# Optimization experiments

Hardware: AMD Instinct MI355X
Metric: run time of the kernel (lower is better)

The kernel has to match this reference:

```python
import jax, jax.numpy as jnp
import numpy as np

B, S, HID = 2, 4096, 768
H, DH = 12, 64
FF = 3072
W = 128  # one-sided attention band; window span = 2*W+1
EPS = 1e-12


def _ln(x, g, b):
    m = jnp.mean(x, axis=-1, keepdims=True)
    v = jnp.var(x, axis=-1, keepdims=True)
    return (x - m) * jax.lax.rsqrt(v + EPS) * g + b


def _band_attend(q, k, v, dmask, w):
    # q,k,v: (B,H,S,D) fp32; dmask: (B,S,2w+1) additive key-mask. Returns (B,S,H,D).
    b, h, s, d = q.shape
    nc = s // w
    qc = q.reshape(b, h, nc, w, d)
    pad = ((0, 0), (0, 0), (w, w), (0, 0))
    kp = jnp.pad(k, pad)
    vp = jnp.pad(v, pad)
    win = jnp.arange(nc)[:, None] * w + jnp.arange(3 * w)[None, :]  # (nc, 3w) indices into padded seq
    kc = kp[:, :, win]  # (B,H,nc,3w,D)
    vc = vp[:, :, win]
    s3 = jnp.einsum('bhcxd,bhcyd->bhcxy', qc, kc)  # (B,H,nc,w,3w)
    # extract band: query i in chunk attends keys j in [i, i+2w] of the 3w window
    off = jnp.arange(w)[:, None] + jnp.arange(2 * w + 1)[None, :]  # (w, 2w+1)
    band = jnp.take_along_axis(s3, off[None, None, None], axis=-1)  # (B,H,nc,w,2w+1)
    band = band.reshape(b, h, s, 2 * w + 1)
    keypos = jnp.arange(s)[:, None] + jnp.arange(-w, w + 1)[None, :]
    valid = (keypos >= 0) & (keypos < s)  # mask_invalid_locations
    band = jnp.where(valid[None, None], band, -1e30)
    band = band + dmask[:, None]
    p = jax.nn.softmax(band, axis=-1)
    # scatter probs back to chunk-dense (w, 3w) layout for the PV matmul
    pc = p.reshape(b, h, nc, w, 2 * w + 1)
    j = jnp.arange(3 * w)[None, :] - jnp.arange(w)[:, None]  # (w,3w) offset indices
    ok = (j >= 0) & (j <= 2 * w)
    jcl = jnp.clip(j, 0, 2 * w)
    pdense = jnp.take_along_axis(pc, jcl[None, None, None], axis=-1)  # (B,H,nc,w,3w)
    pdense = jnp.where(ok[None, None, None], pdense, 0.0)
    ctx = jnp.einsum('bhcxy,bhcyd->bhcxd', pdense, vc)  # (B,H,nc,w,D)
    return ctx.reshape(b, h, s, d).transpose(0, 2, 1, 3)


def setup_inputs() -> dict:
    key = jax.random.key(0)
    ks = jax.random.split(key, 8)
    sc = 0.02
    inp = {
        'hidden_states': jax.random.normal(ks[0], (B, S, HID), jnp.float32),
        'attention_mask': jax.random.randint(ks[1], (B, 1, 1, S), 0, 2, jnp.int32),
        'Wq': jax.random.normal(ks[2], (HID, HID), jnp.float32) * sc,
        'bq': jnp.zeros((HID,), jnp.float32),
        'Wk': jax.random.normal(ks[3], (HID, HID), jnp.float32) * sc,
        'bk': jnp.zeros((HID,), jnp.float32),
        'Wv': jax.random.normal(ks[4], (HID, HID), jnp.float32) * sc,
        'bv': jnp.zeros((HID,), jnp.float32),
        'Wd': jax.random.normal(ks[5], (HID, HID), jnp.float32) * sc,
        'bd': jnp.zeros((HID,), jnp.float32),
        'ln1_g': jnp.ones((HID,), jnp.float32),
        'ln1_b': jnp.zeros((HID,), jnp.float32),
        'Wf': jax.random.normal(ks[6], (HID, FF), jnp.float32) * sc,
        'bf': jnp.zeros((FF,), jnp.float32),
        'Wo': jax.random.normal(ks[7], (FF, HID), jnp.float32) * sc,
        'bo': jnp.zeros((HID,), jnp.float32),
        'ln2_g': jnp.ones((HID,), jnp.float32),
        'ln2_b': jnp.zeros((HID,), jnp.float32),
    }
    return inp


def reference(hidden_states, attention_mask, Wq, bq, Wk, bk, Wv, bv, Wd, bd,
              ln1_g, ln1_b, Wf, bf, Wo, bo, ln2_g, ln2_b):
    def heads(x):
        return x.reshape(B, S, H, DH).transpose(0, 2, 1, 3)  # (B,H,S,DH)

    q = heads(hidden_states @ Wq + bq).astype(jnp.float32) / np.float32(np.sqrt(DH))
    k = heads(hidden_states @ Wk + bk).astype(jnp.float32)
    v = heads(hidden_states @ Wv + bv).astype(jnp.float32)

    am = attention_mask.reshape(B, S)
    maskvals = jnp.where(am != 0, -10000.0, 0.0).astype(jnp.float32)  # (B,S)
    mpad = jnp.pad(maskvals, ((0, 0), (W, W)))
    kidx = jnp.arange(S)[:, None] + jnp.arange(2 * W + 1)[None, :]
    dmask = mpad[:, kidx]  # (B,S,2w+1)

    ctx = _band_attend(q, k, v, dmask, W)  # (B,S,H,DH)

    w_d = Wd.reshape(H, DH, HID)
    proj = jnp.einsum('bfnd,ndh->bfh', ctx, w_d) + bd
    attn_out = _ln(hidden_states + proj, ln1_g, ln1_b)

    ff = jax.nn.gelu(attn_out @ Wf + bf, approximate=False)
    ff = ff @ Wo + bo
    return _ln(ff + attn_out, ln2_g, ln2_b)
```

## Files before the change

### kernel.cpp

```cpp
#include <hip/hip_runtime.h>
#include <cstdint>
#include <cstddef>

#define S_LEN 4096
#define HIDD 768
#define NH 12
#define FFD 3072

typedef float f32x4 __attribute__((ext_vector_type(4)));
typedef short s16x8 __attribute__((ext_vector_type(8)));
typedef short s16x4 __attribute__((ext_vector_type(4)));

__device__ __forceinline__ short f2bf(float f) {
  unsigned u = __float_as_uint(f);
  u += 0x7fffu + ((u >> 16) & 1u);
  return (short)(u >> 16);
}
__device__ __forceinline__ float bf2f(short s) {
  return __uint_as_float(((unsigned)(unsigned short)s) << 16);
}

__device__ __forceinline__ void gload16(const short* g, short* l) {
  __builtin_amdgcn_global_load_lds(
      (__attribute__((address_space(1))) void*)(void*)const_cast<short*>(g),
      (__attribute__((address_space(3))) void*)l, 16, 0, 0);
}

__global__ void convx_k(const float* __restrict__ x, short* __restrict__ o) {
  size_t i = (size_t)blockIdx.x * 256 + threadIdx.x;
  float4 f = ((const float4*)x)[i];
  s16x4 v;
  v[0] = f2bf(f.x); v[1] = f2bf(f.y); v[2] = f2bf(f.z); v[3] = f2bf(f.w);
  ((s16x4*)o)[i] = v;
}

__global__ void wtrans_k(const float* __restrict__ Wq, const float* __restrict__ Wk,
                         const float* __restrict__ Wv, const float* __restrict__ Wd,
                         const float* __restrict__ Wf, const float* __restrict__ Wo,
                         short* __restrict__ oq, short* __restrict__ ok_,
                         short* __restrict__ ov, short* __restrict__ od,
                         short* __restrict__ of_, short* __restrict__ oo) {
  __shared__ float tl[64][65];
  int id = blockIdx.x;
  const float* in; short* out; int R, C, tr, tc;
  if (id < 576) {
    int wsel = id / 144; int t = id % 144; tr = t / 12; tc = t % 12; R = 768; C = 768;
    in = wsel == 0 ? Wq : wsel == 1 ? Wk : wsel == 2 ? Wv : Wd;
    out = wsel == 0 ? oq : wsel == 1 ? ok_ : wsel == 2 ? ov : od;
  } else if (id < 1152) {
    int t = id - 576; tr = t / 48; tc = t % 48; R = 768; C = 3072; in = Wf; out = of_;
  } else {
    int t = id - 1152; tr = t / 12; tc = t % 12; R = 3072; C = 768; in = Wo; out = oo;
  }
  int r0 = tr * 64, c0 = tc * 64;
  int tid = threadIdx.x;
  #pragma unroll
  for (int i = 0; i < 16; i++) {
    int idx = i * 256 + tid; int r = idx >> 6, cc = idx & 63;
    tl[r][cc] = in[(size_t)(r0 + r) * C + c0 + cc];
  }
  __syncthreads();
  #pragma unroll
  for (int i = 0; i < 16; i++) {
    int idx = i * 256 + tid; int cc = idx >> 6, rr = idx & 63;
    out[(size_t)(c0 + cc) * R + r0 + rr] = f2bf(tl[rr][cc]);
  }
}

__global__ void vtrans_k(const short* __restrict__ vh, short* __restrict__ vth) {
  __shared__ short tl[64][72];
  int s0 = blockIdx.x * 64; int bh = blockIdx.y;
  int tid = threadIdx.x;
  const short* base = vh + ((size_t)bh << 18);
  #pragma unroll
  for (int i = 0; i < 16; i++) {
    int idx = i * 256 + tid; int r = idx >> 6, cc = idx & 63;
    tl[r][cc] = base[(size_t)(s0 + r) * 64 + cc];
  }
  __syncthreads();
  short* ob = vth + ((size_t)bh << 18);
  #pragma unroll
  for (int i = 0; i < 16; i++) {
    int idx = i * 256 + tid; int dh = idx >> 6, s = idx & 63;
    ob[((size_t)dh << 12) + s0 + s] = tl[s][dh];
  }
}

template <int EPI, int BN>
__global__ void __launch_bounds__(256) gemm_bt(
    const short* __restrict__ A, const short* __restrict__ Bt,
    const float* __restrict__ bias, const float* __restrict__ bias1,
    const float* __restrict__ bias2, const void* __restrict__ resid,
    void* __restrict__ out, int N, int K) {
  constexpr int NT = BN / 32;
  __shared__ __align__(16) short As[2][128 * 64];
  __shared__ __align__(16) short Bs[2][BN * 64];
  const int tid = threadIdx.x;
  const int lane = tid & 63;
  const int w = tid >> 6;
  const int wr = w >> 1, wc = w & 1;
  const int m0 = blockIdx.x * 128, n0 = blockIdx.y * BN;
  const int lr = lane >> 3;
  const int seg = (lane & 7) ^ lr;
  f32x4 acc[4][NT];
  #pragma unroll
  for (int i = 0; i < 4; i++)
    #pragma unroll
    for (int j = 0; j < NT; j++) { acc[i][j][0] = 0.f; acc[i][j][1] = 0.f; acc[i][j][2] = 0.f; acc[i][j][3] = 0.f; }

  const short* Ab = A + (size_t)(m0 + lr) * K + seg * 8;
  const short* Bb = Bt + (size_t)(n0 + lr) * K + seg * 8;

  auto stage = [&](int buf, int k0) {
    #pragma unroll
    for (int i = 0; i < 4; i++) {
      const int ca = w * 4 + i;
      gload16(Ab + (size_t)(ca * 8) * K + k0, &As[buf][ca * 512]);
    }
    #pragma unroll
    for (int i = 0; i < NT; i++) {
      const int cb = w * NT + i;
      gload16(Bb + (size_t)(cb * 8) * K + k0, &Bs[buf][cb * 512]);
    }
  };

  const int nt_k = K >> 6;
  stage(0, 0);
  __syncthreads();
  int cur = 0;
  for (int t = 0; t < nt_k; ++t) {
    if (t + 1 < nt_k) stage(cur ^ 1, (t + 1) << 6);
    const int kc = (lane >> 4) * 8;
    #pragma unroll
    for (int ks = 0; ks < 2; ks++) {
      const int kb = ks * 32 + kc;
      s16x8 af[4], bfr[NT];
      #pragma unroll
      for (int mt = 0; mt < 4; mt++) {
        const int arow = wr * 64 + mt * 16 + (lane & 15);
        af[mt] = *(const s16x8*)&As[cur][arow * 64 + (kb ^ ((arow & 7) << 3))];
      }
      #pragma unroll
      for (int nt = 0; nt < NT; nt++) {
        const int brow = wc * (BN / 2) + nt * 16 + (lane & 15);
        bfr[nt] = *(const s16x8*)&Bs[cur][brow * 64 + (kb ^ ((brow & 7) << 3))];
      }
      #pragma unroll
      for (int mt = 0; mt < 4; mt++)
        #pragma unroll
        for (int nt = 0; nt < NT; nt++)
          acc[mt][nt] = __builtin_amdgcn_mfma_f32_16x16x32_bf16(af[mt], bfr[nt], acc[mt][nt], 0, 0, 0);
    }
    if (t + 1 < nt_k) {
      __syncthreads();
      cur ^= 1;
    }
  }
  #pragma unroll
  for (int nt = 0; nt < NT; nt++) {
    const int col = n0 + wc * (BN / 2) + nt * 16 + (lane & 15);
    if (EPI == 0) {
      const int cwhich = col >= 1536 ? 2 : (col >= 768 ? 1 : 0);
      const int cwi = col - cwhich * 768;
      const float* bsel = cwhich == 0 ? bias : (cwhich == 1 ? bias1 : bias2);
      const float bvv = bsel[cwi];
      const float sc = (cwhich == 0) ? 0.125f : 1.f;
      const int hh = cwi >> 6, dh = cwi & 63;
      short* outp = (short*)out + (size_t)cwhich * ((size_t)8192 * 768);
      #pragma unroll
      for (int mt = 0; mt < 4; mt++) {
        #pragma unroll
        for (int r = 0; r < 4; r++) {
          const int row = m0 + wr * 64 + mt * 16 + (lane >> 4) * 4 + r;
          const int b = row >> 12, s = row & 4095;
          outp[((((size_t)b * NH + hh) * S_LEN + s) << 6) + dh] = f2bf((acc[mt][nt][r] + bvv) * sc);
        }
      }
    } else {
      const float bvv = bias[col];
      #pragma unroll
      for (int mt = 0; mt < 4; mt++) {
        #pragma unroll
        for (int r = 0; r < 4; r++) {
          const int row = m0 + wr * 64 + mt * 16 + (lane >> 4) * 4 + r;
          float v = acc[mt][nt][r] + bvv;
          if (EPI == 1) {
            float u = 0.7978845608f * v * (1.f + 0.044715f * v * v);
            float e = __expf(2.f * u);
            float th = 1.f - 2.f / (e + 1.f);
            float g = 0.5f * v * (1.f + th);
            ((short*)out)[(size_t)row * N + col] = f2bf(g);
          } else if (EPI == 2) {
            ((float*)out)[(size_t)row * N + col] = v + ((const float*)resid)[(size_t)row * N + col];
          } else {
            ((float*)out)[(size_t)row * N + col] = v + bf2f(((const short*)resid)[(size_t)row * N + col]);
          }
        }
      }
    }
  }
}

__global__ void __launch_bounds__(512, 1) attn_k(
    const short* __restrict__ qh, const short* __restrict__ kh,
    const short* __restrict__ vth, const int* __restrict__ am,
    short* __restrict__ ctx) {
  extern __shared__ char smraw[];
  short* Kb = (short*)smraw;
  float* dmw = (float*)(smraw + 55296);
  short* Pb = (short*)(smraw + 56832);
  const int c = blockIdx.x;
  const int bh = blockIdx.y;
  const int b = bh / NH, hh = bh % NH;
  const int tid = threadIdx.x, lane = tid & 63, w = tid >> 6;
  const int q0 = c * 128, kw0 = q0 - 128;

  for (int ch = tid; ch < 3072; ch += 512) {
    int n = ch >> 3, seg = ch & 7;
    int kp = kw0 + n; kp = kp < 0 ? 0 : (kp > S_LEN - 1 ? S_LEN - 1 : kp);
    *(s16x8*)&Kb[n * 72 + seg * 8] = *(const s16x8*)&kh[(((size_t)bh * S_LEN + kp) << 6) + seg * 8];
  }
  for (int n = tid; n < 384; n += 512) {
    int kp = kw0 + n;
    float d;
    if (kp < 0 || kp >= S_LEN) d = -1e30f;
    else d = (am[b * S_LEN + kp] != 0) ? -10000.f : 0.f;
    dmw[n] = d;
  }
  __syncthreads();

  const short* qrow = qh + ((((size_t)bh * S_LEN) + q0 + w * 16 + (lane & 15)) << 6);
  s16x8 aq0 = *(const s16x8*)&qrow[(lane >> 4) * 8];
  s16x8 aq1 = *(const s16x8*)&qrow[32 + (lane >> 4) * 8];

  f32x4 sacc[24];
  #pragma unroll
  for (int t = 0; t < 24; t++) { sacc[t][0] = 0.f; sacc[t][1] = 0.f; sacc[t][2] = 0.f; sacc[t][3] = 0.f; }
  #pragma unroll
  for (int t = 0; t < 24; t++) {
    const short* kr = &Kb[(t * 16 + (lane & 15)) * 72 + (lane >> 4) * 8];
    s16x8 bk0 = *(const s16x8*)&kr[0];
    s16x8 bk1 = *(const s16x8*)&kr[32];
    sacc[t] = __builtin_amdgcn_mfma_f32_16x16x32_bf16(aq0, bk0, sacc[t], 0, 0, 0);
    sacc[t] = __builtin_amdgcn_mfma_f32_16x16x32_bf16(aq1, bk1, sacc[t], 0, 0, 0);
  }
  const int mbase = w * 16 + (lane >> 4) * 4;
  #pragma unroll
  for (int t = 0; t < 24; t++) {
    int n = t * 16 + (lane & 15);
    float d = dmw[n];
    #pragma unroll
    for (int r = 0; r < 4; r++) {
      int j = n - (mbase + r);
      float sv = sacc[t][r] + d;
      if (j < 0 || j > 256) sv = -1e30f;
      sacc[t][r] = sv;
    }
  }
  short* Pw = Pb + w * 16 * 392;
  #pragma unroll
  for (int r = 0; r < 4; r++) {
    float mx = -3e38f;
    #pragma unroll
    for (int t = 0; t < 24; t++) mx = fmaxf(mx, sacc[t][r]);
    #pragma unroll
    for (int d = 1; d < 16; d <<= 1) mx = fmaxf(mx, __shfl_xor(mx, d));
    float sum = 0.f;
    #pragma unroll
    for (int t = 0; t < 24; t++) { float p = __expf(sacc[t][r] - mx); sacc[t][r] = p; sum += p; }
    #pragma unroll
    for (int d = 1; d < 16; d <<= 1) sum += __shfl_xor(sum, d);
    float inv = 1.f / sum;
    #pragma unroll
    for (int t = 0; t < 24; t++)
      Pw[((lane >> 4) * 4 + r) * 392 + t * 16 + (lane & 15)] = f2bf(sacc[t][r] * inv);
  }
  __syncthreads();

  short* Vt = (short*)smraw;
  for (int ch = tid; ch < 3072; ch += 512) {
    int dh = ch / 48, seg = ch % 48;
    int n0 = seg * 8, kp0 = kw0 + n0;
    const short* vr = vth + (((size_t)bh * 64 + dh) << 12);
    s16x8 vv;
    if (kp0 >= 0 && kp0 + 7 < S_LEN) {
      vv = *(const s16x8*)&vr[kp0];
    } else {
      #pragma unroll
      for (int e = 0; e < 8; e++) {
        int kp = kp0 + e; kp = kp < 0 ? 0 : (kp > S_LEN - 1 ? S_LEN - 1 : kp);
        vv[e] = vr[kp];
      }
    }
    *(s16x8*)&Vt[dh * 392 + n0] = vv;
  }
  __syncthreads();

  f32x4 oacc[4];
  #pragma unroll
  for (int i = 0; i < 4; i++) { oacc[i][0] = 0.f; oacc[i][1] = 0.f; oacc[i][2] = 0.f; oacc[i][3] = 0.f; }
  #pragma unroll
  for (int ksp = 0; ksp < 12; ksp++) {
    s16x8 pa = *(const s16x8*)&Pw[(lane & 15) * 392 + ksp * 32 + (lane >> 4) * 8];
    #pragma unroll
    for (int ct = 0; ct < 4; ct++) {
      s16x8 vb = *(const s16x8*)&Vt[(ct * 16 + (lane & 15)) * 392 + ksp * 32 + (lane >> 4) * 8];
      oacc[ct] = __builtin_amdgcn_mfma_f32_16x16x32_bf16(pa, vb, oacc[ct], 0, 0, 0);
    }
  }
  #pragma unroll
  for (int ct = 0; ct < 4; ct++) {
    #pragma unroll
    for (int r = 0; r < 4; r++) {
      int srow = q0 + w * 16 + (lane >> 4) * 4 + r;
      int col = hh * 64 + ct * 16 + (lane & 15);
      ctx[((size_t)b * S_LEN + srow) * HIDD + col] = f2bf(oacc[ct][r]);
    }
  }
}

template <int OUTBF>
__global__ void ln_k(const float* __restrict__ in, const float* __restrict__ g,
                     const float* __restrict__ bb, void* __restrict__ out) {
  int row = blockIdx.x * 4 + (threadIdx.x >> 6);
  int lane = threadIdx.x & 63;
  const float4* x = (const float4*)(in + (size_t)row * HIDD);
  float4 v0 = x[lane], v1 = x[lane + 64], v2 = x[lane + 128];
  float s = v0.x + v0.y + v0.z + v0.w + v1.x + v1.y + v1.z + v1.w + v2.x + v2.y + v2.z + v2.w;
  float ss = v0.x * v0.x + v0.y * v0.y + v0.z * v0.z + v0.w * v0.w
           + v1.x * v1.x + v1.y * v1.y + v1.z * v1.z + v1.w * v1.w
           + v2.x * v2.x + v2.y * v2.y + v2.z * v2.z + v2.w * v2.w;
  #pragma unroll
  for (int d = 1; d < 64; d <<= 1) { s += __shfl_xor(s, d); ss += __shfl_xor(ss, d); }
  float mean = s * (1.f / 768.f);
  float var = ss * (1.f / 768.f) - mean * mean;
  float rs = rsqrtf(var + 1e-12f);
  const float4* gp = (const float4*)g;
  const float4* bp = (const float4*)bb;
  #pragma unroll
  for (int seg = 0; seg < 3; seg++) {
    int idx = lane + seg * 64;
    float4 vv = seg == 0 ? v0 : seg == 1 ? v1 : v2;
    float4 gg = gp[idx], b4 = bp[idx];
    float o0 = (vv.x - mean) * rs * gg.x + b4.x;
    float o1 = (vv.y - mean) * rs * gg.y + b4.y;
    float o2 = (vv.z - mean) * rs * gg.z + b4.z;
    float o3 = (vv.w - mean) * rs * gg.w + b4.w;
    if (OUTBF) {
      s16x4 o; o[0] = f2bf(o0); o[1] = f2bf(o1); o[2] = f2bf(o2); o[3] = f2bf(o3);
      ((s16x4*)out)[(size_t)row * 192 + idx] = o;
    } else {
      float4 o; o.x = o0; o.y = o1; o.z = o2; o.w = o3;
      ((float4*)out)[(size_t)row * 192 + idx] = o;
    }
  }
}

extern "C" void kernel_launch(void* const* d_in, const int* in_sizes, int n_in,
                              void* d_out, int out_size, void* d_ws, size_t ws_size,
                              hipStream_t stream) {
  const float* hid = (const float*)d_in[0];
  const int* am = (const int*)d_in[1];
  const float* Wq = (const float*)d_in[2];  const float* bq = (const float*)d_in[3];
  const float* Wk = (const float*)d_in[4];  const float* bk = (const float*)d_in[5];
  const float* Wv = (const float*)d_in[6];  const float* bv = (const float*)d_in[7];
  const float* Wd = (const float*)d_in[8];  const float* bd = (const float*)d_in[9];
  const float* g1 = (const float*)d_in[10]; const float* b1 = (const float*)d_in[11];
  const float* Wf = (const float*)d_in[12]; const float* bf = (const float*)d_in[13];
  const float* Wo = (const float*)d_in[14]; const float* bo = (const float*)d_in[15];
  const float* g2 = (const float*)d_in[16]; const float* b2 = (const float*)d_in[17];

  char* ws = (char*)d_ws;
  size_t off = 0;
  auto alloc = [&](size_t bytes) { char* p = ws + off; off += (bytes + 255) & ~(size_t)255; return p; };
  short* Xb   = (short*)alloc((size_t)8192 * 768 * 2);
  short* Wqb  = (short*)alloc((size_t)768 * 768 * 2);
  short* Wkb  = (short*)alloc((size_t)768 * 768 * 2);
  short* Wvb  = (short*)alloc((size_t)768 * 768 * 2);
  short* Wdb  = (short*)alloc((size_t)768 * 768 * 2);
  short* Wfb  = (short*)alloc((size_t)3072 * 768 * 2);
  short* Wob  = (short*)alloc((size_t)768 * 3072 * 2);
  short* qh   = (short*)alloc((size_t)8192 * 768 * 2);
  short* kh   = (short*)alloc((size_t)8192 * 768 * 2);
  short* vh   = (short*)alloc((size_t)8192 * 768 * 2);
  short* vth  = (short*)alloc((size_t)8192 * 768 * 2);
  short* ctx  = (short*)alloc((size_t)8192 * 768 * 2);
  short* aob  = (short*)alloc((size_t)8192 * 768 * 2);
  short* ffb  = (short*)alloc((size_t)8192 * 3072 * 2);
  float* f2r  = (float*)alloc((size_t)8192 * 768 * 4);
  float* ln1in = (float*)d_out;
  (void)vh; (void)kh;

  hipFuncSetAttribute(reinterpret_cast<const void*>(attn_k),
                      hipFuncAttributeMaxDynamicSharedMemorySize, 157184);

  convx_k<<<6144, 256, 0, stream>>>(hid, Xb);
  wtrans_k<<<1728, 256, 0, stream>>>(Wq, Wk, Wv, Wd, Wf, Wo, Wqb, Wkb, Wvb, Wdb, Wfb, Wob);

  gemm_bt<0, 128><<<dim3(64, 18), 256, 0, stream>>>(Xb, Wqb, bq, bk, bv, nullptr, qh, 2304, 768);
  vtrans_k<<<dim3(64, 24), 256, 0, stream>>>(vh, vth);
  attn_k<<<dim3(32, 24), 512, 157184, stream>>>(qh, kh, vth, am, ctx);
  gemm_bt<2, 64><<<dim3(64, 12), 256, 0, stream>>>(ctx, Wdb, bd, nullptr, nullptr, hid, ln1in, 768, 768);
  ln_k<1><<<2048, 256, 0, stream>>>(ln1in, g1, b1, aob);
  gemm_bt<1, 128><<<dim3(64, 24), 256, 0, stream>>>(aob, Wfb, bf, nullptr, nullptr, nullptr, ffb, 3072, 768);
  gemm_bt<3, 64><<<dim3(64, 12), 256, 0, stream>>>(ffb, Wob, bo, nullptr, nullptr, aob, f2r, 768, 3072);
  ln_k<0><<<2048, 256, 0, stream>>>(f2r, g2, b2, d_out);
}
```

Measured before the change: 258.2 us.

## Enlarge GEMM tile to 256 rows, 8 waves, triple-buffered LDS pipeline

The bf16 GEMM kernel grows from 128x BN tiles with 4 waves to 256x BN tiles with 8 waves (512 threads) and moves shared memory to a dynamic buffer. Double buffering becomes a three-stage ring, with loads issued two k-steps ahead and explicit vmcnt waits plus one barrier per step instead of two syncthreads. The aim is to hide global-to-LDS latency and improve operand reuse. The cost is larger LDS use (up to 144KB per block), one block per CU, and half as many blocks, which may hurt occupancy on the smaller GEMMs.

```diff
diff --git a/kernel.cpp b/kernel.cpp
--- a/kernel.cpp
+++ b/kernel.cpp
@@ -87,77 +87,97 @@
 }
 
 template <int EPI, int BN>
-__global__ void __launch_bounds__(256) gemm_bt(
+__global__ void __launch_bounds__(512, 1) gemm_bt(
     const short* __restrict__ A, const short* __restrict__ Bt,
     const float* __restrict__ bias, const float* __restrict__ bias1,
     const float* __restrict__ bias2, const void* __restrict__ resid,
     void* __restrict__ out, int N, int K) {
-  constexpr int NT = BN / 32;
-  __shared__ __align__(16) short As[2][128 * 64];
-  __shared__ __align__(16) short Bs[2][BN * 64];
+  constexpr int BM = 256;
+  constexpr int NT = BN / 64;
+  constexpr int ACH = BM / 64;
+  constexpr int BCH = BN / 64;
+  constexpr int LPI = ACH + BCH;
+  constexpr int ASZ = BM * 64;
+  constexpr int BSZ = BN * 64;
+  extern __shared__ __align__(16) short sm[];
+  short* Abuf = sm;
+  short* Bbuf = sm + 3 * ASZ;
+
   const int tid = threadIdx.x;
   const int lane = tid & 63;
   const int w = tid >> 6;
   const int wr = w >> 1, wc = w & 1;
-  const int m0 = blockIdx.x * 128, n0 = blockIdx.y * BN;
+  const int m0 = blockIdx.x * BM, n0 = blockIdx.y * BN;
   const int lr = lane >> 3;
   const int seg = (lane & 7) ^ lr;
-  f32x4 acc[4][NT];
+
+  constexpr int NT2 = BN / 32;
+  f32x4 acc[4][NT2];
   #pragma unroll
   for (int i = 0; i < 4; i++)
     #pragma unroll
-    for (int j = 0; j < NT; j++) { acc[i][j][0] = 0.f; acc[i][j][1] = 0.f; acc[i][j][2] = 0.f; acc[i][j][3] = 0.f; }
+    for (int j = 0; j < NT2; j++) { acc[i][j][0] = 0.f; acc[i][j][1] = 0.f; acc[i][j][2] = 0.f; acc[i][j][3] = 0.f; }
 
   const short* Ab = A + (size_t)(m0 + lr) * K + seg * 8;
   const short* Bb = Bt + (size_t)(n0 + lr) * K + seg * 8;
 
   auto stage = [&](int buf, int k0) {
     #pragma unroll
-    for (int i = 0; i < 4; i++) {
-      const int ca = w * 4 + i;
-      gload16(Ab + (size_t)(ca * 8) * K + k0, &As[buf][ca * 512]);
-    }
-    #pragma unroll
-    for (int i = 0; i < NT; i++) {
-      const int cb = w * NT + i;
-      gload16(Bb + (size_t)(cb * 8) * K + k0, &Bs[buf][cb * 512]);
+    for (int i = 0; i < ACH; i++) {
+      const int ca = w * ACH + i;
+      gload16(Ab + (size_t)(ca * 8) * K + k0, Abuf + buf * ASZ + ca * 512);
+    }
+    #pragma unroll
+    for (int i = 0; i < BCH; i++) {
+      const int cb = w * BCH + i;
+      gload16(Bb + (size_t)(cb * 8) * K + k0, Bbuf + buf * BSZ + cb * 512);
     }
   };
 
   const int nt_k = K >> 6;
   stage(0, 0);
-  __syncthreads();
+  stage(1, 64);
   int cur = 0;
   for (int t = 0; t < nt_k; ++t) {
-    if (t + 1 < nt_k) stage(cur ^ 1, (t + 1) << 6);
+    if (t + 1 < nt_k) {
+      if constexpr (LPI == 6) asm volatile("s_waitcnt vmcnt(6)" ::: "memory");
+      else                    asm volatile("s_waitcnt vmcnt(5)" ::: "memory");
+    } else {
+      asm volatile("s_waitcnt vmcnt(0)" ::: "memory");
+    }
+    __builtin_amdgcn_s_barrier();
+    asm volatile("" ::: "memory");
+    int nxt = cur + 2; if (nxt >= 3) nxt -= 3;
+    if (t + 2 < nt_k) stage(nxt, (t + 2) << 6);
+
+    const short* Ac = Abuf + cur * ASZ;
+    const short* Bc = Bbuf + cur * BSZ;
     const int kc = (lane >> 4) * 8;
     #pragma unroll
     for (int ks = 0; ks < 2; ks++) {
       const int kb = ks * 32 + kc;
-      s16x8 af[4], bfr[NT];
+      s16x8 af[4], bfr[NT2];
       #pragma unroll
       for (int mt = 0; mt < 4; mt++) {
         const int arow = wr * 64 + mt * 16 + (lane & 15);
-        af[mt] = *(const s16x8*)&As[cur][arow * 64 + (kb ^ ((arow & 7) << 3))];
+        af[mt] = *(const s16x8*)&Ac[arow * 64 + (kb ^ ((arow & 7) << 3))];
       }
       #pragma unroll
-      for (int nt = 0; nt < NT; nt++) {
+      for (int nt = 0; nt < NT2; nt++) {
         const int brow = wc * (BN / 2) + nt * 16 + (lane & 15);
-        bfr[nt] = *(const s16x8*)&Bs[cur][brow * 64 + (kb ^ ((brow & 7) << 3))];
+        bfr[nt] = *(const s16x8*)&Bc[brow * 64 + (kb ^ ((brow & 7) << 3))];
       }
       #pragma unroll
       for (int mt = 0; mt < 4; mt++)
         #pragma unroll
-        for (int nt = 0; nt < NT; nt++)
+        for (int nt = 0; nt < NT2; nt++)
           acc[mt][nt] = __builtin_amdgcn_mfma_f32_16x16x32_bf16(af[mt], bfr[nt], acc[mt][nt], 0, 0, 0);
     }
-    if (t + 1 < nt_k) {
-      __syncthreads();
-      cur ^= 1;
-    }
-  }
-  #pragma unroll
-  for (int nt = 0; nt < NT; nt++) {
+    cur = cur == 2 ? 0 : cur + 1;
+  }
+  (void)NT;
+  #pragma unroll
+  for (int nt = 0; nt < NT2; nt++) {
     const int col = n0 + wc * (BN / 2) + nt * 16 + (lane & 15);
     if (EPI == 0) {
       const int cwhich = col >= 1536 ? 2 : (col >= 768 ? 1 : 0);
@@ -393,16 +413,24 @@
 
   hipFuncSetAttribute(reinterpret_cast<const void*>(attn_k),
                       hipFuncAttributeMaxDynamicSharedMemorySize, 157184);
+  hipFuncSetAttribute(reinterpret_cast<const void*>(&gemm_bt<0, 128>),
+                      hipFuncAttributeMaxDynamicSharedMemorySize, 147456);
+  hipFuncSetAttribute(reinterpret_cast<const void*>(&gemm_bt<1, 128>),
+                      hipFuncAttributeMaxDynamicSharedMemorySize, 147456);
+  hipFuncSetAttribute(reinterpret_cast<const void*>(&gemm_bt<2, 64>),
+                      hipFuncAttributeMaxDynamicSharedMemorySize, 122880);
+  hipFuncSetAttribute(reinterpret_cast<const void*>(&gemm_bt<3, 64>),
+                      hipFuncAttributeMaxDynamicSharedMemorySize, 122880);
 
   convx_k<<<6144, 256, 0, stream>>>(hid, Xb);
   wtrans_k<<<1728, 256, 0, stream>>>(Wq, Wk, Wv, Wd, Wf, Wo, Wqb, Wkb, Wvb, Wdb, Wfb, Wob);
 
-  gemm_bt<0, 128><<<dim3(64, 18), 256, 0, stream>>>(Xb, Wqb, bq, bk, bv, nullptr, qh, 2304, 768);
+  gemm_bt<0, 128><<<dim3(32, 18), 512, 147456, stream>>>(Xb, Wqb, bq, bk, bv, nullptr, qh, 2304, 768);
   vtrans_k<<<dim3(64, 24), 256, 0, stream>>>(vh, vth);
   attn_k<<<dim3(32, 24), 512, 157184, stream>>>(qh, kh, vth, am, ctx);
-  gemm_bt<2, 64><<<dim3(64, 12), 256, 0, stream>>>(ctx, Wdb, bd, nullptr, nullptr, hid, ln1in, 768, 768);
+  gemm_bt<2, 64><<<dim3(32, 12), 512, 122880, stream>>>(ctx, Wdb, bd, nullptr, nullptr, hid, ln1in, 768, 768);
   ln_k<1><<<2048, 256, 0, stream>>>(ln1in, g1, b1, aob);
-  gemm_bt<1, 128><<<dim3(64, 24), 256, 0, stream>>>(aob, Wfb, bf, nullptr, nullptr, nullptr, ffb, 3072, 768);
-  gemm_bt<3, 64><<<dim3(64, 12), 256, 0, stream>>>(ffb, Wob, bo, nullptr, nullptr, aob, f2r, 768, 3072);
+  gemm_bt<1, 128><<<dim3(32, 24), 512, 147456, stream>>>(aob, Wfb, bf, nullptr, nullptr, nullptr, ffb, 3072, 768);
+  gemm_bt<3, 64><<<dim3(32, 12), 512, 122880, stream>>>(ffb, Wob, bo, nullptr, nullptr, aob, f2r, 768, 3072);
   ln_k<0><<<2048, 256, 0, stream>>>(f2r, g2, b2, d_out);
 }
```

New measurement: 271.7 us. 5.2% more time.

## Add 256x256 eight-wave ping-pong GEMM for QKV and FFN-up projections

Applied to the files above, without the earlier changes.

Adds a new GEMM kernel with 256x256 output tiles, 512 threads, double-buffered LDS filled by direct global-to-LDS loads, and a quadrant-by-quadrant MFMA schedule that interleaves LDS reads and next-tile staging with s_setprio and barriers. The block index is remapped so consecutive tiles land on the same XCD, aiming at better L2 reuse. It replaces the older 128-row gemm_bt for the QKV projection and for the GELU FFN-up GEMM, cutting global and LDS traffic per FLOP. In exchange the grids are small (288 and 384 blocks, one per CU), and 128 KB of LDS plus many accumulator registers limit occupancy.

```diff
diff --git a/kernel.cpp b/kernel.cpp
--- a/kernel.cpp
+++ b/kernel.cpp
@@ -86,11 +86,189 @@
   }
 }
 
+template <int QM, int QN>
+__device__ __forceinline__ void mmac(f32x4 (&acc)[8][4], const s16x8 (&af)[4][2],
+                                     const s16x8 (&bf)[2][2]) {
+  #pragma unroll
+  for (int ks = 0; ks < 2; ks++)
+    #pragma unroll
+    for (int mt = 0; mt < 4; mt++)
+      #pragma unroll
+      for (int nt = 0; nt < 2; nt++)
+        acc[QM * 4 + mt][QN * 2 + nt] = __builtin_amdgcn_mfma_f32_16x16x32_bf16(
+            af[mt][ks], bf[nt][ks], acc[QM * 4 + mt][QN * 2 + nt], 0, 0, 0);
+}
+
+template <int EPI>
+__global__ void __launch_bounds__(512, 1) gemm8p(
+    const short* __restrict__ A, const short* __restrict__ Bt,
+    const float* __restrict__ bias, const float* __restrict__ bias1,
+    const float* __restrict__ bias2, void* __restrict__ out, int N, int K,
+    int MB) {
+  extern __shared__ __align__(16) short sm[];
+  constexpr int TSZ = 256 * 64;
+  short* Abase = sm;
+  short* Bbase = sm + 2 * TSZ;
+
+  const int tid = threadIdx.x;
+  const int lane = tid & 63;
+  const int w = tid >> 6;
+  const int wr = w >> 2, wc = w & 3;
+  const int lm = lane & 15, lk = lane >> 4;
+
+  const int nwg = gridDim.x;
+  const int bid = blockIdx.x;
+  const int q = nwg >> 3, r = nwg & 7;
+  const int xcd = bid & 7, idx = bid >> 3;
+  const int wg = (xcd < r ? xcd * (q + 1) : r * (q + 1) + (xcd - r) * q) + idx;
+  const int mb = wg % MB, nb = wg / MB;
+  const int m0 = mb * 256, n0 = nb * 256;
+
+  const int lr = lane >> 3;
+  const int seg = (lane & 7) ^ lr;
+
+  f32x4 acc[8][4];
+  #pragma unroll
+  for (int i = 0; i < 8; i++)
+    #pragma unroll
+    for (int j = 0; j < 4; j++) { acc[i][j][0] = 0.f; acc[i][j][1] = 0.f; acc[i][j][2] = 0.f; acc[i][j][3] = 0.f; }
+
+  const short* Ag = A + (size_t)(m0 + lr) * K + seg * 8;
+  const short* Bg = Bt + (size_t)(n0 + lr) * K + seg * 8;
+
+  auto stageA = [&](int d, int k0) {
+    #pragma unroll
+    for (int i = 0; i < 4; i++) {
+      const int c = w * 4 + i;
+      gload16(Ag + (size_t)(c * 8) * K + k0, Abase + d * TSZ + c * 512);
+    }
+  };
+  auto stageB = [&](int d, int k0) {
+    #pragma unroll
+    for (int i = 0; i < 4; i++) {
+      const int c = w * 4 + i;
+      gload16(Bg + (size_t)(c * 8) * K + k0, Bbase + d * TSZ + c * 512);
+    }
+  };
+  auto readA = [&](s16x8 (&dst)[4][2], int d, int qm) {
+    #pragma unroll
+    for (int mt = 0; mt < 4; mt++) {
+      const int ar = wr * 128 + qm * 64 + mt * 16 + lm;
+      #pragma unroll
+      for (int ks = 0; ks < 2; ks++) {
+        const int sg = (ks * 4 + lk) ^ (ar & 7);
+        dst[mt][ks] = *(const s16x8*)&Abase[d * TSZ + ar * 64 + sg * 8];
+      }
+    }
+  };
+  auto readB = [&](s16x8 (&dst)[2][2], int d, int qn) {
+    #pragma unroll
+    for (int nt = 0; nt < 2; nt++) {
+      const int br = wc * 64 + qn * 32 + nt * 16 + lm;
+      #pragma unroll
+      for (int ks = 0; ks < 2; ks++) {
+        const int sg = (ks * 4 + lk) ^ (br & 7);
+        dst[nt][ks] = *(const s16x8*)&Bbase[d * TSZ + br * 64 + sg * 8];
+      }
+    }
+  };
+
+  const int nk = K >> 6;
+  stageA(0, 0); stageB(0, 0);
+  asm volatile("s_waitcnt vmcnt(0)" ::: "memory");
+  __builtin_amdgcn_sched_barrier(0);
+  __builtin_amdgcn_s_barrier();
+
+  s16x8 afA[4][2], bf0[2][2], bf1[2][2];
+  for (int j = 0; j < nk; ++j) {
+    const int cur = j & 1;
+    const bool more = (j + 1 < nk);
+    readA(afA, cur, 0);
+    readB(bf0, cur, 0);
+    if (more) stageA(cur ^ 1, (j + 1) << 6);
+    __builtin_amdgcn_s_barrier();
+    asm volatile("s_waitcnt lgkmcnt(0)" ::: "memory");
+    __builtin_amdgcn_sched_barrier(0);
+    __builtin_amdgcn_s_setprio(1);
+    mmac<0, 0>(acc, afA, bf0);
+    __builtin_amdgcn_s_setprio(0);
+    __builtin_amdgcn_s_barrier();
+    readB(bf1, cur, 1);
+    if (more) stageB(cur ^ 1, (j + 1) << 6);
+    __builtin_amdgcn_s_barrier();
+    asm volatile("s_waitcnt lgkmcnt(0)" ::: "memory");
+    __builtin_amdgcn_sched_barrier(0);
+    __builtin_amdgcn_s_setprio(1);
+    mmac<0, 1>(acc, afA, bf1);
+    __builtin_amdgcn_s_setprio(0);
+    __builtin_amdgcn_s_barrier();
+    readA(afA, cur, 1);
+    __builtin_amdgcn_s_barrier();
+    asm volatile("s_waitcnt lgkmcnt(0)" ::: "memory");
+    __builtin_amdgcn_sched_barrier(0);
+    __builtin_amdgcn_s_setprio(1);
+    mmac<1, 1>(acc, afA, bf1);
+    __builtin_amdgcn_s_setprio(0);
+    __builtin_amdgcn_s_barrier();
+    __builtin_amdgcn_s_setprio(1);
+    mmac<1, 0>(acc, afA, bf0);
+    __builtin_amdgcn_s_setprio(0);
+    if (more) {
+      asm volatile("s_waitcnt vmcnt(0)" ::: "memory");
+      __builtin_amdgcn_sched_barrier(0);
+    }
+    __builtin_amdgcn_s_barrier();
+  }
+
+  #pragma unroll
+  for (int qm = 0; qm < 2; qm++) {
+    #pragma unroll
+    for (int qn = 0; qn < 2; qn++) {
+      #pragma unroll
+      for (int nt = 0; nt < 2; nt++) {
+        const int col = n0 + wc * 64 + qn * 32 + nt * 16 + lm;
+        if (EPI == 0) {
+          const int cwhich = col >= 1536 ? 2 : (col >= 768 ? 1 : 0);
+          const int cwi = col - cwhich * 768;
+          const float* bsel = cwhich == 0 ? bias : (cwhich == 1 ? bias1 : bias2);
+          const float bvv = bsel[cwi];
+          const float sc = (cwhich == 0) ? 0.125f : 1.f;
+          const int hh = cwi >> 6, dh = cwi & 63;
+          short* outp = (short*)out + (size_t)cwhich * ((size_t)8192 * 768);
+          #pragma unroll
+          for (int mt = 0; mt < 4; mt++) {
+            #pragma unroll
+            for (int rr = 0; rr < 4; rr++) {
+              const int row = m0 + wr * 128 + qm * 64 + mt * 16 + lk * 4 + rr;
+              const int b = row >> 12, s = row & 4095;
+              outp[((((size_t)b * NH + hh) * S_LEN + s) << 6) + dh] =
+                  f2bf((acc[qm * 4 + mt][qn * 2 + nt][rr] + bvv) * sc);
+            }
+          }
+        } else {
+          const float bvv = bias[col];
+          #pragma unroll
+          for (int mt = 0; mt < 4; mt++) {
+            #pragma unroll
+            for (int rr = 0; rr < 4; rr++) {
+              const int row = m0 + wr * 128 + qm * 64 + mt * 16 + lk * 4 + rr;
+              float v = acc[qm * 4 + mt][qn * 2 + nt][rr] + bvv;
+              float u = 0.7978845608f * v * (1.f + 0.044715f * v * v);
+              float e = __expf(2.f * u);
+              float th = 1.f - 2.f / (e + 1.f);
+              ((short*)out)[(size_t)row * N + col] = f2bf(0.5f * v * (1.f + th));
+            }
+          }
+        }
+      }
+    }
+  }
+}
+
 template <int EPI, int BN>
 __global__ void __launch_bounds__(256) gemm_bt(
     const short* __restrict__ A, const short* __restrict__ Bt,
-    const float* __restrict__ bias, const float* __restrict__ bias1,
-    const float* __restrict__ bias2, const void* __restrict__ resid,
+    const float* __restrict__ bias, const void* __restrict__ resid,
     void* __restrict__ out, int N, int K) {
   constexpr int NT = BN / 32;
   __shared__ __align__(16) short As[2][128 * 64];
@@ -151,50 +329,22 @@
         for (int nt = 0; nt < NT; nt++)
           acc[mt][nt] = __builtin_amdgcn_mfma_f32_16x16x32_bf16(af[mt], bfr[nt], acc[mt][nt], 0, 0, 0);
     }
-    if (t + 1 < nt_k) {
-      __syncthreads();
-      cur ^= 1;
-    }
+    if (t + 1 < nt_k) { __syncthreads(); cur ^= 1; }
   }
   #pragma unroll
   for (int nt = 0; nt < NT; nt++) {
     const int col = n0 + wc * (BN / 2) + nt * 16 + (lane & 15);
-    if (EPI == 0) {
-      const int cwhich = col >= 1536 ? 2 : (col >= 768 ? 1 : 0);
-      const int cwi = col - cwhich * 768;
-      const float* bsel = cwhich == 0 ? bias : (cwhich == 1 ? bias1 : bias2);
-      const float bvv = bsel[cwi];
-      const float sc = (cwhich == 0) ? 0.125f : 1.f;
-      const int hh = cwi >> 6, dh = cwi & 63;
-      short* outp = (short*)out + (size_t)cwhich * ((size_t)8192 * 768);
-      #pragma unroll
-      for (int mt = 0; mt < 4; mt++) {
-        #pragma unroll
-        for (int r = 0; r < 4; r++) {
-          const int row = m0 + wr * 64 + mt * 16 + (lane >> 4) * 4 + r;
-          const int b = row >> 12, s = row & 4095;
-          outp[((((size_t)b * NH + hh) * S_LEN + s) << 6) + dh] = f2bf((acc[mt][nt][r] + bvv) * sc);
-        }
-      }
-    } else {
-      const float bvv = bias[col];
-      #pragma unroll
-      for (int mt = 0; mt < 4; mt++) {
-        #pragma unroll
-        for (int r = 0; r < 4; r++) {
-          const int row = m0 + wr * 64 + mt * 16 + (lane >> 4) * 4 + r;
-          float v = acc[mt][nt][r] + bvv;
-          if (EPI == 1) {
-            float u = 0.7978845608f * v * (1.f + 0.044715f * v * v);
-            float e = __expf(2.f * u);
-            float th = 1.f - 2.f / (e + 1.f);
-            float g = 0.5f * v * (1.f + th);
-            ((short*)out)[(size_t)row * N + col] = f2bf(g);
-          } else if (EPI == 2) {
-            ((float*)out)[(size_t)row * N + col] = v + ((const float*)resid)[(size_t)row * N + col];
-          } else {
-            ((float*)out)[(size_t)row * N + col] = v + bf2f(((const short*)resid)[(size_t)row * N + col]);
-          }
+    const float bvv = bias[col];
+    #pragma unroll
+    for (int mt = 0; mt < 4; mt++) {
+      #pragma unroll
+      for (int rr = 0; rr < 4; rr++) {
+        const int row = m0 + wr * 64 + mt * 16 + (lane >> 4) * 4 + rr;
+        float v = acc[mt][nt][rr] + bvv;
+        if (EPI == 2) {
+          ((float*)out)[(size_t)row * N + col] = v + ((const float*)resid)[(size_t)row * N + col];
+        } else {
+          ((float*)out)[(size_t)row * N + col] = v + bf2f(((const short*)resid)[(size_t)row * N + col]);
         }
       }
     }
@@ -393,16 +543,20 @@
 
   hipFuncSetAttribute(reinterpret_cast<const void*>(attn_k),
                       hipFuncAttributeMaxDynamicSharedMemorySize, 157184);
+  hipFuncSetAttribute(reinterpret_cast<const void*>(&gemm8p<0>),
+                      hipFuncAttributeMaxDynamicSharedMemorySize, 131072);
+  hipFuncSetAttribute(reinterpret_cast<const void*>(&gemm8p<1>),
+                      hipFuncAttributeMaxDynamicSharedMemorySize, 131072);
 
   convx_k<<<6144, 256, 0, stream>>>(hid, Xb);
   wtrans_k<<<1728, 256, 0, stream>>>(Wq, Wk, Wv, Wd, Wf, Wo, Wqb, Wkb, Wvb, Wdb, Wfb, Wob);
 
-  gemm_bt<0, 128><<<dim3(64, 18), 256, 0, stream>>>(Xb, Wqb, bq, bk, bv, nullptr, qh, 2304, 768);
+  gemm8p<0><<<288, 512, 131072, stream>>>(Xb, Wqb, bq, bk, bv, qh, 2304, 768, 32);
   vtrans_k<<<dim3(64, 24), 256, 0, stream>>>(vh, vth);
   attn_k<<<dim3(32, 24), 512, 157184, stream>>>(qh, kh, vth, am, ctx);
-  gemm_bt<2, 64><<<dim3(64, 12), 256, 0, stream>>>(ctx, Wdb, bd, nullptr, nullptr, hid, ln1in, 768, 768);
+  gemm_bt<2, 64><<<dim3(64, 12), 256, 0, stream>>>(ctx, Wdb, bd, hid, ln1in, 768, 768);
   ln_k<1><<<2048, 256, 0, stream>>>(ln1in, g1, b1, aob);
-  gemm_bt<1, 128><<<dim3(64, 24), 256, 0, stream>>>(aob, Wfb, bf, nullptr, nullptr, nullptr, ffb, 3072, 768);
-  gemm_bt<3, 64><<<dim3(64, 12), 256, 0, stream>>>(ffb, Wob, bo, nullptr, nullptr, aob, f2r, 768, 3072);
+  gemm8p<1><<<384, 512, 131072, stream>>>(aob, Wfb, bf, nullptr, nullptr, ffb, 3072, 768, 32);
+  gemm_bt<3, 64><<<dim3(64, 12), 256, 0, stream>>>(ffb, Wob, bo, aob, f2r, 768, 3072);
   ln_k<0><<<2048, 256, 0, stream>>>(f2r, g2, b2, d_out);
 }
```

Result: slower. 275.4 us (+6.7%).
